# Kernel optimization log

Hardware: AMD Instinct MI355X
Metric: run time of the kernel (lower is better)

Reference implementation:

```python
import jax, jax.numpy as jnp
import numpy as np

D_MODEL = 1024
N_HEADS = 16
D_K = D_MODEL // N_HEADS


def setup_inputs() -> dict:
    key = jax.random.key(0)
    ks = jax.random.split(key, 10)
    B, S = 4, 2048
    scale = 1.0 / np.sqrt(D_MODEL)
    inp = {
        "x": jax.random.normal(ks[0], (B, S, D_MODEL), dtype=jnp.float32),
        "mask": jnp.ones((B, S), dtype=jnp.int32),
        "w_q": jax.random.normal(ks[1], (D_MODEL, D_MODEL), dtype=jnp.float32) * scale,
        "b_q": jnp.zeros((D_MODEL,), dtype=jnp.float32),
        "w_k": jax.random.normal(ks[2], (D_MODEL, D_MODEL), dtype=jnp.float32) * scale,
        "b_k": jnp.zeros((D_MODEL,), dtype=jnp.float32),
        "w_v": jax.random.normal(ks[3], (D_MODEL, D_MODEL), dtype=jnp.float32) * scale,
        "b_v": jnp.zeros((D_MODEL,), dtype=jnp.float32),
        "w_o": jax.random.normal(ks[4], (D_MODEL, D_MODEL), dtype=jnp.float32) * scale,
        "b_o": jnp.zeros((D_MODEL,), dtype=jnp.float32),
    }
    return inp


def reference(x, mask, w_q, b_q, w_k, b_k, w_v, b_v, w_o, b_o):
    B, S, _ = x.shape
    # projections; weights stored (in, out) so x @ W + b
    def proj(w, b):
        return (x @ w + b).reshape(B, S, N_HEADS, D_K).transpose(0, 2, 1, 3)  # [B,H,S,Dk]
    Q = proj(w_q, b_q)
    K = proj(w_k, b_k)
    V = proj(w_v, b_v)
    scores = jnp.einsum("bhqd,bhkd->bhqk", Q, K) / np.sqrt(D_K)  # [B,H,S,S]
    # mask: (B,S) -> (B,1,1,S); masked positions set to -1e9 (matches masked_fill)
    scores = jnp.where(mask[:, None, None, :] == 0, jnp.float32(-1e9), scores)
    attn = jax.nn.softmax(scores, axis=-1)
    # dropout is identity at inference (eval mode)
    context = jnp.einsum("bhqk,bhkd->bhqd", attn, V)  # [B,H,S,Dk]
    context = context.transpose(0, 2, 1, 3).reshape(B, S, D_MODEL)
    return context @ w_o + b_o
```

## Files before the change

kernel.cpp:

```cpp
#include <hip/hip_runtime.h>

typedef __attribute__((ext_vector_type(8)))  short short8;
typedef __attribute__((ext_vector_type(4)))  float f32x4;
typedef __attribute__((ext_vector_type(16))) float f32x16;

__device__ __forceinline__ short f2b(float f) {
    union { float f; unsigned u; } v; v.f = f;
    unsigned r = v.u + 0x7FFF + ((v.u >> 16) & 1);
    return (short)(r >> 16);
}

__device__ __forceinline__ float fexp2(float x) {
    float r;
    asm("v_exp_f32 %0, %1" : "=v"(r) : "v"(x));
    return r;
}

__device__ __forceinline__ void gll16(const void* g, void* l) {
    __builtin_amdgcn_global_load_lds(
        (const __attribute__((address_space(1))) void*)g,
        (__attribute__((address_space(3))) void*)l, 16, 0, 0);
}


__global__ __launch_bounds__(256) void xconv_kernel(const float4* __restrict__ X,
                                                    short* __restrict__ xb) {
    int i = blockIdx.x * 256 + threadIdx.x;
    float4 v = X[i];
    short4 o;
    o.x = f2b(v.x); o.y = f2b(v.y); o.z = f2b(v.z); o.w = f2b(v.w);
    ((short4*)xb)[i] = o;
}

__global__ __launch_bounds__(256) void wconv_kernel(const float* __restrict__ W,
                                                    short* __restrict__ WT, int row_off) {
    __shared__ float t[32][33];
    int bx = blockIdx.x, by = blockIdx.y;
    int c = threadIdx.x & 31, r0 = threadIdx.x >> 5;
    #pragma unroll
    for (int p = 0; p < 4; ++p) {
        int r = r0 + p * 8;
        t[r][c] = W[(size_t)(by * 32 + r) * 1024 + bx * 32 + c];
    }
    __syncthreads();
    #pragma unroll
    for (int p = 0; p < 4; ++p) {
        int r = r0 + p * 8;
        WT[(size_t)(row_off + bx * 32 + r) * 1024 + by * 32 + c] = f2b(t[c][r]);
    }
}

__global__ __launch_bounds__(256) void vtrans_kernel(const short* __restrict__ V,
                                                     short* __restrict__ Vt) {
    __shared__ short t[64][72];
    int st = blockIdx.x, bh = blockIdx.y;
    const size_t vbase = (size_t)bh * 2048 * 64;
    const size_t tbase = (size_t)bh * 64 * 2048;
    int tid = threadIdx.x;
    #pragma unroll
    for (int p = 0; p < 16; ++p) {
        int e = p * 256 + tid;
        int r = e >> 6, c = e & 63;
        t[r][c] = V[vbase + (size_t)(st * 64 + r) * 64 + c];
    }
    __syncthreads();
    #pragma unroll
    for (int p = 0; p < 16; ++p) {
        int e = p * 256 + tid;
        int d = e >> 6, c = e & 63;
        Vt[tbase + (size_t)d * 2048 + st * 64 + c] = t[c][d];
    }
}

__global__ __launch_bounds__(256) void mfma_gemm_kernel(
    const short* __restrict__ A, const short* __restrict__ Bt,
    const float* __restrict__ bias,
    short* __restrict__ Qo, short* __restrict__ Ko, short* __restrict__ Vo,
    float* __restrict__ Co, int K, int mode)
{
    __shared__ __align__(16) short As[2][128 * 32];
    __shared__ __align__(16) short Bs[2][128 * 32];

    const int tid = threadIdx.x;
    const int lane = tid & 63;
    const int w = tid >> 6;
    const int quad = lane >> 4;
    const int l15 = lane & 15;
    const int wm = (w & 1) * 64;
    const int wn = (w >> 1) * 64;
    const int m0 = blockIdx.y * 128;
    const int n0 = blockIdx.x * 128;

    const int rl = lane >> 2;
    const int cl = lane & 3;
    const short* srcA[2]; const short* srcB[2];
    int doff[2];
    #pragma unroll
    for (int t = 0; t < 2; ++t) {
        int row = w * 32 + t * 16 + rl;
        int sc = cl ^ (row & 3);
        srcA[t] = A  + (size_t)(m0 + row) * K + sc * 8;
        srcB[t] = Bt + (size_t)(n0 + row) * K + sc * 8;
        doff[t] = (w * 32 + t * 16) * 32;
    }

    int offA[4], offB[4];
    #pragma unroll
    for (int i = 0; i < 4; ++i) {
        int m = wm + i * 16 + l15;
        offA[i] = m * 32 + ((quad ^ (m & 3)) * 8);
        int n = wn + i * 16 + l15;
        offB[i] = n * 32 + ((quad ^ (n & 3)) * 8);
    }

    f32x4 acc[4][4];
    #pragma unroll
    for (int i = 0; i < 4; ++i)
        #pragma unroll
        for (int j = 0; j < 4; ++j)
            acc[i][j] = (f32x4){0.f, 0.f, 0.f, 0.f};

    #pragma unroll
    for (int t = 0; t < 2; ++t) {
        gll16(srcA[t], As[0] + doff[t]);
        gll16(srcB[t], Bs[0] + doff[t]);
    }
    __syncthreads();

    const int KT = K >> 5;
    for (int kt = 0; kt < KT; ++kt) {
        if (kt + 1 < KT) {
            int k1 = (kt + 1) << 5;
            int nb = (kt + 1) & 1;
            #pragma unroll
            for (int t = 0; t < 2; ++t) {
                gll16(srcA[t] + k1, As[nb] + doff[t]);
                gll16(srcB[t] + k1, Bs[nb] + doff[t]);
            }
        }
        const short* as = As[kt & 1];
        const short* bs = Bs[kt & 1];
        short8 af[4], bfr[4];
        #pragma unroll
        for (int i = 0; i < 4; ++i) af[i] = *(const short8*)(as + offA[i]);
        #pragma unroll
        for (int j = 0; j < 4; ++j) bfr[j] = *(const short8*)(bs + offB[j]);
        #pragma unroll
        for (int i = 0; i < 4; ++i)
            #pragma unroll
            for (int j = 0; j < 4; ++j)
                acc[i][j] = __builtin_amdgcn_mfma_f32_16x16x32_bf16(af[i], bfr[j], acc[i][j], 0, 0, 0);
        __syncthreads();
    }

    #pragma unroll
    for (int j = 0; j < 4; ++j) {
        int ng = n0 + wn + j * 16 + l15;
        float bv = bias[ng];
        if (mode == 0) {
            int mat = ng >> 10;
            int nl = ng & 1023;
            short* dst = (mat == 0) ? Qo : (mat == 1) ? Ko : Vo;
            float scl = (mat == 0) ? 0.18033688011112042f : 1.0f;
            int hh = nl >> 6, dd = nl & 63;
            #pragma unroll
            for (int i = 0; i < 4; ++i)
                #pragma unroll
                for (int r = 0; r < 4; ++r) {
                    int mg = m0 + wm + i * 16 + quad * 4 + r;
                    int bb = mg >> 11, ss = mg & 2047;
                    dst[(((size_t)(bb * 16 + hh)) * 2048 + ss) * 64 + dd] = f2b((acc[i][j][r] + bv) * scl);
                }
        } else {
            #pragma unroll
            for (int i = 0; i < 4; ++i)
                #pragma unroll
                for (int r = 0; r < 4; ++r) {
                    int mg = m0 + wm + i * 16 + quad * 4 + r;
                    Co[(size_t)mg * 1024 + ng] = acc[i][j][r] + bv;
                }
        }
    }
}

__global__ __launch_bounds__(256) void attn_mfma_kernel(
    const short* __restrict__ Q, const short* __restrict__ Kg,
    const short* __restrict__ Vt, const int* __restrict__ mask,
    short* __restrict__ ctx)
{
    __shared__ __align__(16) short Qs[128 * 64];
    __shared__ __align__(16) short Ks[2][64 * 64];
    __shared__ __align__(16) short Vs[2][64 * 64];
    __shared__ int msks[2][64];
    __shared__ float Linv[4][32];

    const int tid = threadIdx.x;
    const int lane = tid & 63;
    const int w = tid >> 6;
    const int l31 = lane & 31;
    const int hi = lane >> 5;
    const int q0 = blockIdx.x * 128;
    const int h = blockIdx.y;
    const int b = blockIdx.z;
    const int bh = b * 16 + h;
    const size_t qkbase = (size_t)bh * 2048 * 64;
    const size_t vtbase = (size_t)bh * 64 * 2048;

    const int rl8 = lane >> 3;
    const int cl8 = lane & 7;

    #pragma unroll
    for (int t = 0; t < 4; ++t) {
        int row = w * 32 + t * 8 + rl8;
        int sc = cl8 ^ (row & 7);
        gll16(Q + qkbase + (size_t)(q0 + row) * 64 + sc * 8, Qs + (w * 32 + t * 8) * 64);
    }

    const short* srcK[2]; const short* srcV[2];
    int dstoff[2];
    #pragma unroll
    for (int t = 0; t < 2; ++t) {
        int row = w * 16 + t * 8 + rl8;
        int sc = cl8 ^ (row & 7);
        srcK[t] = Kg + qkbase + (size_t)row * 64 + sc * 8;
        srcV[t] = Vt + vtbase + (size_t)row * 2048 + sc * 8;
        dstoff[t] = (w * 16 + t * 8) * 64;
    }

    #pragma unroll
    for (int t = 0; t < 2; ++t) {
        gll16(srcK[t], Ks[0] + dstoff[t]);
        gll16(srcV[t], Vs[0] + dstoff[t]);
    }
    if (tid < 64) msks[0][tid] = mask[b * 2048 + tid];

    __syncthreads();

    short8 qf[4];
    const int qr = w * 32 + l31;
    #pragma unroll
    for (int s = 0; s < 4; ++s)
        qf[s] = *(const short8*)(Qs + qr * 64 + (((s << 1) | hi) ^ (qr & 7)) * 8);

    f32x16 o[2];
    #pragma unroll
    for (int ch = 0; ch < 2; ++ch)
        #pragma unroll
        for (int r = 0; r < 16; ++r) o[ch][r] = 0.f;
    float lsum = 0.f;

    for (int t = 0; t < 32; ++t) {
        const int bidx = t & 1;
        if (t + 1 < 32) {
            const int nb = (t + 1) & 1;
            const int kt1 = (t + 1) * 64;
            #pragma unroll
            for (int s = 0; s < 2; ++s) {
                gll16(srcK[s] + (size_t)kt1 * 64, Ks[nb] + dstoff[s]);
                gll16(srcV[s] + kt1, Vs[nb] + dstoff[s]);
            }
            if (tid < 64) msks[nb][tid] = mask[b * 2048 + kt1 + tid];
        }

        const short* ks = Ks[bidx];
        const short* vs = Vs[bidx];
        unsigned long long bz = __ballot(msks[bidx][tid & 63] == 0);

        #pragma unroll
        for (int km = 0; km < 2; ++km) {
            f32x16 sa;
            #pragma unroll
            for (int r = 0; r < 16; ++r) sa[r] = 0.f;
            const int kr = km * 32 + l31;
            #pragma unroll
            for (int s = 0; s < 4; ++s) {
                short8 ka = *(const short8*)(ks + kr * 64 + (((s << 1) | hi) ^ (l31 & 7)) * 8);
                sa = __builtin_amdgcn_mfma_f32_32x32x16_bf16(ka, qf[s], sa, 0, 0, 0);
            }
            float ps[16];
            #pragma unroll
            for (int r = 0; r < 16; ++r) ps[r] = fexp2(sa[r]);
            if (bz) {
                #pragma unroll
                for (int r = 0; r < 16; ++r) {
                    int key = km * 32 + (r & 3) + 8 * (r >> 2) + 4 * hi;
                    if (msks[bidx][key] == 0) ps[r] = 0.f;
                }
            }
            #pragma unroll
            for (int r = 0; r < 16; ++r) lsum += ps[r];

            unsigned pk[8];
            #pragma unroll
            for (int c = 0; c < 8; ++c) {
                unsigned u0 = __builtin_bit_cast(unsigned, ps[2 * c])     + 0x8000u;
                unsigned u1 = __builtin_bit_cast(unsigned, ps[2 * c + 1]) + 0x8000u;
                pk[c] = __builtin_amdgcn_perm(u1, u0, 0x07060302u);
            }
            unsigned sk[8];
            #pragma unroll
            for (int c = 0; c < 8; ++c) sk[c] = (unsigned)__shfl_xor((int)pk[c], 32);

            uint4 A1u, A2u;
            A1u.x = hi ? sk[2] : pk[0];
            A1u.y = hi ? sk[3] : pk[1];
            A1u.z = hi ? pk[2] : sk[0];
            A1u.w = hi ? pk[3] : sk[1];
            A2u.x = hi ? sk[6] : pk[4];
            A2u.y = hi ? sk[7] : pk[5];
            A2u.z = hi ? pk[6] : sk[4];
            A2u.w = hi ? pk[7] : sk[5];
            short8 A1 = __builtin_bit_cast(short8, A1u);
            short8 A2 = __builtin_bit_cast(short8, A2u);

            #pragma unroll
            for (int ch = 0; ch < 2; ++ch) {
                const int d = ch * 32 + l31;
                short8 vb0 = *(const short8*)(vs + d * 64 + (((km * 4) | hi) ^ (d & 7)) * 8);
                short8 vb1 = *(const short8*)(vs + d * 64 + (((km * 4 + 2) | hi) ^ (d & 7)) * 8);
                o[ch] = __builtin_amdgcn_mfma_f32_32x32x16_bf16(A1, vb0, o[ch], 0, 0, 0);
                o[ch] = __builtin_amdgcn_mfma_f32_32x32x16_bf16(A2, vb1, o[ch], 0, 0, 0);
            }
        }
        __syncthreads();
    }

    float ltot = lsum + __shfl_xor(lsum, 32);
    if (hi == 0) Linv[w][l31] = 1.0f / ltot;
    asm volatile("s_waitcnt lgkmcnt(0)" ::: "memory");
    float invr[16];
    #pragma unroll
    for (int r = 0; r < 16; ++r)
        invr[r] = Linv[w][(r & 3) + 8 * (r >> 2) + 4 * hi];
    #pragma unroll
    for (int ch = 0; ch < 2; ++ch)
        #pragma unroll
        for (int r = 0; r < 16; ++r) {
            int rowq = (r & 3) + 8 * (r >> 2) + 4 * hi;
            int qg = q0 + w * 32 + rowq;
            ctx[((size_t)b * 2048 + qg) * 1024 + h * 64 + ch * 32 + l31] =
                f2b(o[ch][r] * invr[r]);
        }
}


extern "C" void kernel_launch(void* const* d_in, const int* in_sizes, int n_in,
                              void* d_out, int out_size, void* d_ws, size_t ws_size,
                              hipStream_t stream) {
    const size_t ME = (size_t)8192 * 1024;

    char* ws = (char*)d_ws;
    short* xb    = (short*)ws; ws += ME * 2;
    short* wqkvt = (short*)ws; ws += (size_t)3072 * 1024 * 2;
    short* wot   = (short*)ws; ws += (size_t)1024 * 1024 * 2;
    float* bqkv  = (float*)ws; ws += 3072 * 4;
    short* Qb    = (short*)ws; ws += ME * 2;
    short* Kb    = (short*)ws; ws += ME * 2;
    short* Vb    = (short*)ws; ws += ME * 2;
    short* Vt    = (short*)ws; ws += ME * 2;

    xconv_kernel<<<8192, 256, 0, stream>>>((const float4*)d_in[0], xb);
    wconv_kernel<<<dim3(32, 32), 256, 0, stream>>>((const float*)d_in[2], wqkvt, 0);
    wconv_kernel<<<dim3(32, 32), 256, 0, stream>>>((const float*)d_in[4], wqkvt, 1024);
    wconv_kernel<<<dim3(32, 32), 256, 0, stream>>>((const float*)d_in[6], wqkvt, 2048);
    wconv_kernel<<<dim3(32, 32), 256, 0, stream>>>((const float*)d_in[8], wot, 0);
    hipMemcpyAsync(bqkv,        d_in[3], 4096, hipMemcpyDeviceToDevice, stream);
    hipMemcpyAsync(bqkv + 1024, d_in[5], 4096, hipMemcpyDeviceToDevice, stream);
    hipMemcpyAsync(bqkv + 2048, d_in[7], 4096, hipMemcpyDeviceToDevice, stream);

    mfma_gemm_kernel<<<dim3(24, 64), 256, 0, stream>>>(
        xb, wqkvt, bqkv, Qb, Kb, Vb, nullptr, 1024, 0);

    vtrans_kernel<<<dim3(32, 64), 256, 0, stream>>>(Vb, Vt);

    attn_mfma_kernel<<<dim3(16, 16, 4), 256, 0, stream>>>(
        Qb, Kb, Vt, (const int*)d_in[1], xb );

    mfma_gemm_kernel<<<dim3(8, 64), 256, 0, stream>>>(
        xb, wot, (const float*)d_in[9], nullptr, nullptr, nullptr, (float*)d_out, 1024, 1);
}
```

Before: 346.4 us.

## Merge weight conversions, drop bias copies, load Q directly, reorder attention grid

```diff
diff --git a/kernel.cpp b/kernel.cpp
--- a/kernel.cpp
+++ b/kernel.cpp
@@ -32,9 +32,15 @@
     ((short4*)xb)[i] = o;
 }
 
-__global__ __launch_bounds__(256) void wconv_kernel(const float* __restrict__ W,
-                                                    short* __restrict__ WT, int row_off) {
+__global__ __launch_bounds__(256) void wconv4_kernel(
+    const float* __restrict__ w0, const float* __restrict__ w1,
+    const float* __restrict__ w2, const float* __restrict__ w3,
+    short* __restrict__ wqkvt, short* __restrict__ wot) {
     __shared__ float t[32][33];
+    int z = blockIdx.z;
+    const float* W = (z == 0) ? w0 : (z == 1) ? w1 : (z == 2) ? w2 : w3;
+    short* WT = (z < 3) ? wqkvt : wot;
+    int row_off = (z < 3) ? z * 1024 : 0;
     int bx = blockIdx.x, by = blockIdx.y;
     int c = threadIdx.x & 31, r0 = threadIdx.x >> 5;
     #pragma unroll
@@ -74,7 +80,8 @@
 
 __global__ __launch_bounds__(256) void mfma_gemm_kernel(
     const short* __restrict__ A, const short* __restrict__ Bt,
-    const float* __restrict__ bias,
+    const float* __restrict__ b0, const float* __restrict__ b1,
+    const float* __restrict__ b2,
     short* __restrict__ Qo, short* __restrict__ Ko, short* __restrict__ Vo,
     float* __restrict__ Co, int K, int mode)
 {
@@ -156,10 +163,10 @@
     #pragma unroll
     for (int j = 0; j < 4; ++j) {
         int ng = n0 + wn + j * 16 + l15;
-        float bv = bias[ng];
         if (mode == 0) {
             int mat = ng >> 10;
             int nl = ng & 1023;
+            float bv = (mat == 0) ? b0[nl] : (mat == 1) ? b1[nl] : b2[nl];
             short* dst = (mat == 0) ? Qo : (mat == 1) ? Ko : Vo;
             float scl = (mat == 0) ? 0.18033688011112042f : 1.0f;
             int hh = nl >> 6, dd = nl & 63;
@@ -172,6 +179,7 @@
                     dst[(((size_t)(bb * 16 + hh)) * 2048 + ss) * 64 + dd] = f2b((acc[i][j][r] + bv) * scl);
                 }
         } else {
+            float bv = b0[ng];
             #pragma unroll
             for (int i = 0; i < 4; ++i)
                 #pragma unroll
@@ -188,7 +196,6 @@
     const short* __restrict__ Vt, const int* __restrict__ mask,
     short* __restrict__ ctx)
 {
-    __shared__ __align__(16) short Qs[128 * 64];
     __shared__ __align__(16) short Ks[2][64 * 64];
     __shared__ __align__(16) short Vs[2][64 * 64];
     __shared__ int msks[2][64];
@@ -199,22 +206,15 @@
     const int w = tid >> 6;
     const int l31 = lane & 31;
     const int hi = lane >> 5;
-    const int q0 = blockIdx.x * 128;
-    const int h = blockIdx.y;
-    const int b = blockIdx.z;
-    const int bh = b * 16 + h;
+    const int bh = blockIdx.x;
+    const int q0 = blockIdx.y * 128;
+    const int h = bh & 15;
+    const int b = bh >> 4;
     const size_t qkbase = (size_t)bh * 2048 * 64;
     const size_t vtbase = (size_t)bh * 64 * 2048;
 
     const int rl8 = lane >> 3;
     const int cl8 = lane & 7;
-
-    #pragma unroll
-    for (int t = 0; t < 4; ++t) {
-        int row = w * 32 + t * 8 + rl8;
-        int sc = cl8 ^ (row & 7);
-        gll16(Q + qkbase + (size_t)(q0 + row) * 64 + sc * 8, Qs + (w * 32 + t * 8) * 64);
-    }
 
     const short* srcK[2]; const short* srcV[2];
     int dstoff[2];
@@ -234,13 +234,13 @@
     }
     if (tid < 64) msks[0][tid] = mask[b * 2048 + tid];
 
-    __syncthreads();
-
     short8 qf[4];
-    const int qr = w * 32 + l31;
-    #pragma unroll
-    for (int s = 0; s < 4; ++s)
-        qf[s] = *(const short8*)(Qs + qr * 64 + (((s << 1) | hi) ^ (qr & 7)) * 8);
+    {
+        const short* qptr = Q + qkbase + (size_t)(q0 + w * 32 + l31) * 64;
+        #pragma unroll
+        for (int s = 0; s < 4; ++s)
+            qf[s] = *(const short8*)(qptr + (((s << 1) | hi)) * 8);
+    }
 
     f32x16 o[2];
     #pragma unroll
@@ -248,6 +248,8 @@
         #pragma unroll
         for (int r = 0; r < 16; ++r) o[ch][r] = 0.f;
     float lsum = 0.f;
+
+    __syncthreads();
 
     for (int t = 0; t < 32; ++t) {
         const int bidx = t & 1;
@@ -353,29 +355,26 @@
     short* xb    = (short*)ws; ws += ME * 2;
     short* wqkvt = (short*)ws; ws += (size_t)3072 * 1024 * 2;
     short* wot   = (short*)ws; ws += (size_t)1024 * 1024 * 2;
-    float* bqkv  = (float*)ws; ws += 3072 * 4;
     short* Qb    = (short*)ws; ws += ME * 2;
     short* Kb    = (short*)ws; ws += ME * 2;
     short* Vb    = (short*)ws; ws += ME * 2;
     short* Vt    = (short*)ws; ws += ME * 2;
 
     xconv_kernel<<<8192, 256, 0, stream>>>((const float4*)d_in[0], xb);
-    wconv_kernel<<<dim3(32, 32), 256, 0, stream>>>((const float*)d_in[2], wqkvt, 0);
-    wconv_kernel<<<dim3(32, 32), 256, 0, stream>>>((const float*)d_in[4], wqkvt, 1024);
-    wconv_kernel<<<dim3(32, 32), 256, 0, stream>>>((const float*)d_in[6], wqkvt, 2048);
-    wconv_kernel<<<dim3(32, 32), 256, 0, stream>>>((const float*)d_in[8], wot, 0);
-    hipMemcpyAsync(bqkv,        d_in[3], 4096, hipMemcpyDeviceToDevice, stream);
-    hipMemcpyAsync(bqkv + 1024, d_in[5], 4096, hipMemcpyDeviceToDevice, stream);
-    hipMemcpyAsync(bqkv + 2048, d_in[7], 4096, hipMemcpyDeviceToDevice, stream);
+    wconv4_kernel<<<dim3(32, 32, 4), 256, 0, stream>>>(
+        (const float*)d_in[2], (const float*)d_in[4],
+        (const float*)d_in[6], (const float*)d_in[8], wqkvt, wot);
 
     mfma_gemm_kernel<<<dim3(24, 64), 256, 0, stream>>>(
-        xb, wqkvt, bqkv, Qb, Kb, Vb, nullptr, 1024, 0);
+        xb, wqkvt, (const float*)d_in[3], (const float*)d_in[5], (const float*)d_in[7],
+        Qb, Kb, Vb, nullptr, 1024, 0);
 
     vtrans_kernel<<<dim3(32, 64), 256, 0, stream>>>(Vb, Vt);
 
-    attn_mfma_kernel<<<dim3(16, 16, 4), 256, 0, stream>>>(
+    attn_mfma_kernel<<<dim3(64, 16), 256, 0, stream>>>(
         Qb, Kb, Vt, (const int*)d_in[1], xb );
 
     mfma_gemm_kernel<<<dim3(8, 64), 256, 0, stream>>>(
-        xb, wot, (const float*)d_in[9], nullptr, nullptr, nullptr, (float*)d_out, 1024, 1);
-}
+        xb, wot, (const float*)d_in[9], nullptr, nullptr,
+        nullptr, nullptr, nullptr, (float*)d_out, 1024, 1);
+}
```

Result: no change. 339.9 us (-1.9%).
